# Kernel tuning notes

Hardware: AMD Instinct MI355X
Metric: run time of the kernel (lower is better)

The kernel has to match this reference:

```python
import jax, jax.numpy as jnp
import numpy as np

N_DATA = 12288
N_QUERY = 12288
DIM = 3
RADIUS = 0.085  # gives ~32 neighbors/query for uniform points in [0,1]^3


def setup_inputs() -> dict:
    key = jax.random.key(0)
    k1, k2 = jax.random.split(key)
    data = jax.random.uniform(k1, (N_DATA, DIM), dtype=jnp.float32)
    queries = jax.random.uniform(k2, (N_QUERY, DIM), dtype=jnp.float32)
    radius = jnp.float32(RADIUS)
    return {"data": data, "queries": queries, "radius": radius}


def reference(data, queries, radius):
    # Dense, jit-compatible equivalent of KDTree.query_radius with return_distance=True.
    # Original returns ragged CSR (neighbors_index, neighbors_row_splits, weights=dists**2).
    # Fixed-shape encoding: boolean membership mask [M, N] (row m, col n True iff
    # data[n] is a neighbor of queries[m]; CSR indices = nonzero cols in row order),
    # row_splits [M+1] (exact CSR splits), and dense weights [M, N] = squared
    # distance where within radius else 0 (CSR weights = masked entries in row order).
    sq_d = jnp.sum(data * data, axis=-1)          # [N]
    sq_q = jnp.sum(queries * queries, axis=-1)    # [M]
    # ||q - d||^2 = ||q||^2 + ||d||^2 - 2 q.d  (GEMM form)
    d2 = sq_q[:, None] + sq_d[None, :] - 2.0 * (queries @ data.T)  # [M, N]
    d2 = jnp.maximum(d2, 0.0)
    mask = d2 <= radius * radius                  # [M, N]
    counts = jnp.sum(mask, axis=-1, dtype=jnp.int32)  # [M]
    row_splits = jnp.concatenate(
        [jnp.zeros((1,), jnp.int32), jnp.cumsum(counts)]
    )  # [M+1], matches nbr_dict['neighbors_row_splits']
    weights = jnp.where(mask, d2, 0.0)            # dists**2, masked
    return row_splits, mask, weights
```

## Files before the change

### kernel.cpp

```cpp
#include <hip/hip_runtime.h>


#define TILE 1024

__global__ __launch_bounds__(256) void nbr_kernel(
    const float* __restrict__ data,
    const float* __restrict__ queries,
    const float* __restrict__ radius_p,
    float* __restrict__ out,
    int* __restrict__ counts,
    int N, long long mask_off, long long w_off)
{
    __shared__ __align__(16) float tile[TILE * 3 + 4];

    const int m = blockIdx.x;
    const int tid = threadIdx.x;

    const float r = radius_p[0];
    const float r2 = __fmul_rn(r, r);
    const float q0 = queries[3 * m + 0];
    const float q1 = queries[3 * m + 1];
    const float q2 = queries[3 * m + 2];
    const float sq_q = __fadd_rn(
        __fadd_rn(__fmul_rn(q0, q0), __fmul_rn(q1, q1)), __fmul_rn(q2, q2));

    float* mask_row = out + mask_off + (long long)m * N;
    float* w_row    = out + w_off    + (long long)m * N;

    int cnt = 0;

    auto compute = [&](float d0, float d1, float d2e, float& mv, float& wv) -> int {
        const float sq_d = __fadd_rn(
            __fadd_rn(__fmul_rn(d0, d0), __fmul_rn(d1, d1)), __fmul_rn(d2e, d2e));
        const float dot = __fmaf_rn(q2, d2e, __fmaf_rn(q1, d1, __fmul_rn(q0, d0)));
        const float s = __fadd_rn(sq_q, sq_d);
        float v = __fmaf_rn(-2.0f, dot, s);
        v = fmaxf(v, 0.0f);
        const bool in = (v <= r2);
        mv = in ? 1.0f : 0.0f;
        wv = in ? v : 0.0f;
        return in ? 1 : 0;
    };

    constexpr int NQ = (TILE - 16) / 4;

    for (int tb = 0; tb < N; tb += TILE) {
        __syncthreads();
        {
            const float4* src = reinterpret_cast<const float4*>(data + 3LL * tb);
            #pragma unroll
            for (int k = 0; k < 3 * TILE / 4 / 256; ++k) {
                const int f = k * 256 + tid;
                const float4 v = src[f];
                const int w = 4 * f + 3;
                tile[w + 0] = v.x;
                tile[w + 1] = v.y;
                tile[w + 2] = v.z;
                tile[w + 3] = v.w;
            }
        }
        __syncthreads();

        if (tid < 16) {
            const int n = (tid < 15) ? tid : (TILE - 1);
            float mv, wv;
            cnt += compute(tile[3 * n + 3], tile[3 * n + 4], tile[3 * n + 5], mv, wv);
            mask_row[tb + n] = mv;
            w_row[tb + n] = wv;
        }

        if (tid < NQ) {
            const int c = tid;
            const float4 A = *reinterpret_cast<const float4*>(&tile[48 + 12 * c]);
            const float4 B = *reinterpret_cast<const float4*>(&tile[52 + 12 * c]);
            const float4 C = *reinterpret_cast<const float4*>(&tile[56 + 12 * c]);
            float4 mv, wv;
            cnt += compute(A.x, A.y, A.z, mv.x, wv.x);
            cnt += compute(A.w, B.x, B.y, mv.y, wv.y);
            cnt += compute(B.z, B.w, C.x, mv.z, wv.z);
            cnt += compute(C.y, C.z, C.w, mv.w, wv.w);
            const long long g = (long long)tb + 15 + 4 * c;
            *reinterpret_cast<float4*>(mask_row + g) = mv;
            *reinterpret_cast<float4*>(w_row + g) = wv;
        }
    }

    for (int off = 32; off > 0; off >>= 1) cnt += __shfl_down(cnt, off);
    __shared__ int lds_cnt;
    if (tid == 0) lds_cnt = 0;
    __syncthreads();
    if ((tid & 63) == 0) atomicAdd(&lds_cnt, cnt);
    __syncthreads();
    if (tid == 0) counts[m] = lds_cnt;
}

__global__ __launch_bounds__(256) void nbr_kernel_generic(
    const float* __restrict__ data,
    const float* __restrict__ queries,
    const float* __restrict__ radius_p,
    float* __restrict__ out,
    int* __restrict__ counts,
    int N, long long mask_off, long long w_off)
{
    const int m = blockIdx.x;
    const int tid = threadIdx.x;
    const float r = radius_p[0];
    const float r2 = __fmul_rn(r, r);
    const float q0 = queries[3 * m + 0], q1 = queries[3 * m + 1], q2 = queries[3 * m + 2];
    const float sq_q = __fadd_rn(
        __fadd_rn(__fmul_rn(q0, q0), __fmul_rn(q1, q1)), __fmul_rn(q2, q2));
    float* mask_row = out + mask_off + (long long)m * N;
    float* w_row    = out + w_off    + (long long)m * N;
    int cnt = 0;
    for (int n = tid; n < N; n += 256) {
        const float d0 = data[3 * n], d1 = data[3 * n + 1], d2e = data[3 * n + 2];
        const float sq_d = __fadd_rn(
            __fadd_rn(__fmul_rn(d0, d0), __fmul_rn(d1, d1)), __fmul_rn(d2e, d2e));
        const float dot = __fmaf_rn(q2, d2e, __fmaf_rn(q1, d1, __fmul_rn(q0, d0)));
        float v = __fmaf_rn(-2.0f, dot, __fadd_rn(sq_q, sq_d));
        v = fmaxf(v, 0.0f);
        const bool in = (v <= r2);
        mask_row[n] = in ? 1.0f : 0.0f;
        w_row[n] = in ? v : 0.0f;
        cnt += in ? 1 : 0;
    }
    for (int off = 32; off > 0; off >>= 1) cnt += __shfl_down(cnt, off);
    __shared__ int lds_cnt;
    if (tid == 0) lds_cnt = 0;
    __syncthreads();
    if ((tid & 63) == 0) atomicAdd(&lds_cnt, cnt);
    __syncthreads();
    if (tid == 0) counts[m] = lds_cnt;
}

__global__ __launch_bounds__(256) void scan_kernel(
    const int* __restrict__ counts, float* __restrict__ out, int M)
{
    __shared__ int sums[256];
    const int t = threadIdx.x;
    const int CH = (M + 255) / 256;
    const int base = t * CH;

    int local[64];
    int s = 0;
    for (int i = 0; i < CH; ++i) {
        const int v = (base + i < M) ? counts[base + i] : 0;
        local[i] = v;
        s += v;
    }
    sums[t] = s;
    __syncthreads();
    for (int off = 1; off < 256; off <<= 1) {
        const int v = (t >= off) ? sums[t - off] : 0;
        __syncthreads();
        sums[t] += v;
        __syncthreads();
    }
    int prefix = sums[t] - s;
    for (int i = 0; i < CH; ++i) {
        if (base + i < M) out[base + i] = (float)prefix;
        prefix += local[i];
    }
    if (t == 255) out[M] = (float)prefix;
}

extern "C" void kernel_launch(void* const* d_in, const int* in_sizes, int n_in,
                              void* d_out, int out_size, void* d_ws, size_t ws_size,
                              hipStream_t stream) {
    const float* data    = (const float*)d_in[0];
    const float* queries = (const float*)d_in[1];
    const float* radius  = (const float*)d_in[2];

    const int N = in_sizes[0] / 3;
    const int M = in_sizes[1] / 3;

    float* out = (float*)d_out;
    int* counts = (int*)d_ws;

    const long long mask_off = (long long)M + 1;
    const long long w_off = mask_off + (long long)M * N;

    const bool fast = (N % TILE == 0) && (M % 16 == 0) && (N % 16 == 0);
    if (fast) {
        nbr_kernel<<<M, 256, 0, stream>>>(data, queries, radius, out, counts,
                                          N, mask_off, w_off);
    } else {
        nbr_kernel_generic<<<M, 256, 0, stream>>>(data, queries, radius, out,
                                                  counts, N, mask_off, w_off);
    }
    scan_kernel<<<1, 256, 0, stream>>>(counts, out, M);
}
```

Before: 1.259 ms.

## Split into nontemporal zero-fill plus sparse scatter of in-radius hits

```diff
diff --git a/kernel.cpp b/kernel.cpp
--- a/kernel.cpp
+++ b/kernel.cpp
@@ -1,9 +1,34 @@
 #include <hip/hip_runtime.h>
 
 
-#define TILE 1024
-
-__global__ __launch_bounds__(256) void nbr_kernel(
+#define ZGRID 2048
+#define RPB 8
+#define DTILE 1024
+
+typedef float floatx4 __attribute__((ext_vector_type(4)));
+
+__global__ __launch_bounds__(256) void zero_kernel(
+    float* __restrict__ out, long long start, long long count)
+{
+    const int head = (int)((4 - (start & 3)) & 3);
+    const long long qstart = start + head;
+    const long long K = (count - head) >> 2;
+    const int tail = (int)((count - head) & 3);
+
+    floatx4* __restrict__ base = reinterpret_cast<floatx4*>(out + qstart);
+    const floatx4 z = {0.f, 0.f, 0.f, 0.f};
+    const long long stride = (long long)gridDim.x * 256;
+    for (long long i = (long long)blockIdx.x * 256 + threadIdx.x; i < K; i += stride)
+        __builtin_nontemporal_store(z, base + i);
+
+    if (blockIdx.x == 0 && (int)threadIdx.x < head + tail) {
+        const int t = threadIdx.x;
+        const long long e = (t < head) ? (start + t) : (qstart + 4 * K + (t - head));
+        out[e] = 0.0f;
+    }
+}
+
+__global__ __launch_bounds__(256) void sparse_kernel(
     const float* __restrict__ data,
     const float* __restrict__ queries,
     const float* __restrict__ radius_p,
@@ -11,87 +36,77 @@
     int* __restrict__ counts,
     int N, long long mask_off, long long w_off)
 {
-    __shared__ __align__(16) float tile[TILE * 3 + 4];
-
-    const int m = blockIdx.x;
+    __shared__ float tile[DTILE * 3];
+    __shared__ int red[RPB][4];
+
+    const int m0 = blockIdx.x * RPB;
     const int tid = threadIdx.x;
 
     const float r = radius_p[0];
     const float r2 = __fmul_rn(r, r);
-    const float q0 = queries[3 * m + 0];
-    const float q1 = queries[3 * m + 1];
-    const float q2 = queries[3 * m + 2];
-    const float sq_q = __fadd_rn(
-        __fadd_rn(__fmul_rn(q0, q0), __fmul_rn(q1, q1)), __fmul_rn(q2, q2));
-
-    float* mask_row = out + mask_off + (long long)m * N;
-    float* w_row    = out + w_off    + (long long)m * N;
-
-    int cnt = 0;
-
-    auto compute = [&](float d0, float d1, float d2e, float& mv, float& wv) -> int {
-        const float sq_d = __fadd_rn(
-            __fadd_rn(__fmul_rn(d0, d0), __fmul_rn(d1, d1)), __fmul_rn(d2e, d2e));
-        const float dot = __fmaf_rn(q2, d2e, __fmaf_rn(q1, d1, __fmul_rn(q0, d0)));
-        const float s = __fadd_rn(sq_q, sq_d);
-        float v = __fmaf_rn(-2.0f, dot, s);
-        v = fmaxf(v, 0.0f);
-        const bool in = (v <= r2);
-        mv = in ? 1.0f : 0.0f;
-        wv = in ? v : 0.0f;
-        return in ? 1 : 0;
-    };
-
-    constexpr int NQ = (TILE - 16) / 4;
-
-    for (int tb = 0; tb < N; tb += TILE) {
+
+    float qx[RPB], qy[RPB], qz[RPB], qs[RPB];
+    long long moff[RPB], woff[RPB];
+    #pragma unroll
+    for (int j = 0; j < RPB; ++j) {
+        const float q0 = queries[3 * (m0 + j) + 0];
+        const float q1 = queries[3 * (m0 + j) + 1];
+        const float q2 = queries[3 * (m0 + j) + 2];
+        qx[j] = q0; qy[j] = q1; qz[j] = q2;
+        qs[j] = __fadd_rn(
+            __fadd_rn(__fmul_rn(q0, q0), __fmul_rn(q1, q1)), __fmul_rn(q2, q2));
+        moff[j] = mask_off + (long long)(m0 + j) * N;
+        woff[j] = w_off    + (long long)(m0 + j) * N;
+    }
+    int cnt[RPB];
+    #pragma unroll
+    for (int j = 0; j < RPB; ++j) cnt[j] = 0;
+
+    for (int tb = 0; tb < N; tb += DTILE) {
         __syncthreads();
         {
             const float4* src = reinterpret_cast<const float4*>(data + 3LL * tb);
+            float4* dst = reinterpret_cast<float4*>(tile);
             #pragma unroll
-            for (int k = 0; k < 3 * TILE / 4 / 256; ++k) {
-                const int f = k * 256 + tid;
-                const float4 v = src[f];
-                const int w = 4 * f + 3;
-                tile[w + 0] = v.x;
-                tile[w + 1] = v.y;
-                tile[w + 2] = v.z;
-                tile[w + 3] = v.w;
+            for (int k = 0; k < DTILE * 3 / 4 / 256; ++k)
+                dst[k * 256 + tid] = src[k * 256 + tid];
+        }
+        __syncthreads();
+
+        #pragma unroll
+        for (int e = 0; e < DTILE / 256; ++e) {
+            const int lo = e * 256 + tid;
+            const int n = tb + lo;
+            const float d0 = tile[3 * lo + 0];
+            const float d1 = tile[3 * lo + 1];
+            const float d2 = tile[3 * lo + 2];
+            const float sqd = __fadd_rn(
+                __fadd_rn(__fmul_rn(d0, d0), __fmul_rn(d1, d1)), __fmul_rn(d2, d2));
+            #pragma unroll
+            for (int j = 0; j < RPB; ++j) {
+                const float dot = __fmaf_rn(qz[j], d2,
+                                   __fmaf_rn(qy[j], d1, __fmul_rn(qx[j], d0)));
+                float v = __fmaf_rn(-2.0f, dot, __fadd_rn(qs[j], sqd));
+                v = fmaxf(v, 0.0f);
+                if (v <= r2) {
+                    out[moff[j] + n] = 1.0f;
+                    out[woff[j] + n] = v;
+                    ++cnt[j];
+                }
             }
         }
-        __syncthreads();
-
-        if (tid < 16) {
-            const int n = (tid < 15) ? tid : (TILE - 1);
-            float mv, wv;
-            cnt += compute(tile[3 * n + 3], tile[3 * n + 4], tile[3 * n + 5], mv, wv);
-            mask_row[tb + n] = mv;
-            w_row[tb + n] = wv;
-        }
-
-        if (tid < NQ) {
-            const int c = tid;
-            const float4 A = *reinterpret_cast<const float4*>(&tile[48 + 12 * c]);
-            const float4 B = *reinterpret_cast<const float4*>(&tile[52 + 12 * c]);
-            const float4 C = *reinterpret_cast<const float4*>(&tile[56 + 12 * c]);
-            float4 mv, wv;
-            cnt += compute(A.x, A.y, A.z, mv.x, wv.x);
-            cnt += compute(A.w, B.x, B.y, mv.y, wv.y);
-            cnt += compute(B.z, B.w, C.x, mv.z, wv.z);
-            cnt += compute(C.y, C.z, C.w, mv.w, wv.w);
-            const long long g = (long long)tb + 15 + 4 * c;
-            *reinterpret_cast<float4*>(mask_row + g) = mv;
-            *reinterpret_cast<float4*>(w_row + g) = wv;
-        }
-    }
-
-    for (int off = 32; off > 0; off >>= 1) cnt += __shfl_down(cnt, off);
-    __shared__ int lds_cnt;
-    if (tid == 0) lds_cnt = 0;
-    __syncthreads();
-    if ((tid & 63) == 0) atomicAdd(&lds_cnt, cnt);
-    __syncthreads();
-    if (tid == 0) counts[m] = lds_cnt;
+    }
+
+    const int wave = tid >> 6, lane = tid & 63;
+    #pragma unroll
+    for (int j = 0; j < RPB; ++j) {
+        int c = cnt[j];
+        for (int off = 32; off > 0; off >>= 1) c += __shfl_down(c, off);
+        if (lane == 0) red[j][wave] = c;
+    }
+    __syncthreads();
+    if (tid < RPB)
+        counts[m0 + tid] = red[tid][0] + red[tid][1] + red[tid][2] + red[tid][3];
 }
 
 __global__ __launch_bounds__(256) void nbr_kernel_generic(
@@ -106,7 +121,7 @@
     const int tid = threadIdx.x;
     const float r = radius_p[0];
     const float r2 = __fmul_rn(r, r);
-    const float q0 = queries[3 * m + 0], q1 = queries[3 * m + 1], q2 = queries[3 * m + 2];
+    const float q0 = queries[3 * m], q1 = queries[3 * m + 1], q2 = queries[3 * m + 2];
     const float sq_q = __fadd_rn(
         __fadd_rn(__fmul_rn(q0, q0), __fmul_rn(q1, q1)), __fmul_rn(q2, q2));
     float* mask_row = out + mask_off + (long long)m * N;
@@ -180,10 +195,11 @@
     const long long mask_off = (long long)M + 1;
     const long long w_off = mask_off + (long long)M * N;
 
-    const bool fast = (N % TILE == 0) && (M % 16 == 0) && (N % 16 == 0);
-    if (fast) {
-        nbr_kernel<<<M, 256, 0, stream>>>(data, queries, radius, out, counts,
-                                          N, mask_off, w_off);
+    if ((M % RPB == 0) && (N % DTILE == 0) &&
+        ws_size >= (size_t)M * sizeof(int)) {
+        zero_kernel<<<ZGRID, 256, 0, stream>>>(out, mask_off, 2LL * M * N);
+        sparse_kernel<<<M / RPB, 256, 0, stream>>>(data, queries, radius, out,
+                                                   counts, N, mask_off, w_off);
     } else {
         nbr_kernel_generic<<<M, 256, 0, stream>>>(data, queries, radius, out,
                                                   counts, N, mask_off, w_off);
```

Measured after the change: 1.463 ms. 1.16x slower.
